# Kernel tuning notes

Measured on AMD Instinct MI355X. Metric: run time of the kernel, lower is better.

## Reference

```python
import jax, jax.numpy as jnp
import numpy as np

CODEBOOK_SIZE = 1024
CODEBOOK_DIM = 64
COMMITMENT_WEIGHT = 0.25
DECAY = 0.99
EPS = 1e-5


def setup_inputs() -> dict:
    key = jax.random.key(0)
    k1, k2, k3 = jax.random.split(key, 3)
    B, D, T = 32, CODEBOOK_DIM, 4096
    z = jax.random.normal(k1, (B, D, T), dtype=jnp.float32)
    embedding = jax.random.normal(k2, (CODEBOOK_SIZE, CODEBOOK_DIM), dtype=jnp.float32)
    cluster_size = jnp.zeros((CODEBOOK_SIZE,), dtype=jnp.float32)
    embed_avg = jax.random.normal(k3, (CODEBOOK_SIZE, CODEBOOK_DIM), dtype=jnp.float32)
    return {"z": z, "embedding": embedding, "cluster_size": cluster_size, "embed_avg": embed_avg}


def reference(z, embedding, cluster_size, embed_avg):
    # z: [B, D, T]; embedding/embed_avg: [K, D]; cluster_size: [K]
    B, D, T = z.shape
    K = embedding.shape[0]
    z_flat = jnp.transpose(z, (0, 2, 1)).reshape(-1, D)  # [N, D], N = B*T

    # squared-euclidean distances via expansion (matches torch cdist expansion)
    dist = (
        jnp.sum(z_flat * z_flat, axis=1, keepdims=True)
        + jnp.sum(embedding * embedding, axis=1)
        - 2.0 * (z_flat @ embedding.T)
    )  # [N, K]
    indices = jnp.argmin(dist, axis=1)  # [N] int

    # EMA updates (training path). one_hot.sum(0) -> segment count; one_hot.T @ z_flat -> segment sum
    counts = jax.ops.segment_sum(jnp.ones(z_flat.shape[0], dtype=z_flat.dtype), indices, num_segments=K)
    new_cluster_size = cluster_size * DECAY + (1.0 - DECAY) * counts
    embed_sum = jax.ops.segment_sum(z_flat, indices, num_segments=K)  # [K, D]
    new_embed_avg = embed_avg * DECAY + (1.0 - DECAY) * embed_sum
    n = jnp.sum(new_cluster_size)
    smoothed = (new_cluster_size + EPS) / (n + K * EPS) * n  # Laplace smoothing
    new_embedding = new_embed_avg / smoothed[:, None]  # [K, D]

    # quantize with the *updated* codebook (as in the torch in-place update)
    z_q_flat = new_embedding[indices]  # [N, D] gather
    loss = COMMITMENT_WEIGHT * jnp.mean((z_flat - jax.lax.stop_gradient(z_q_flat)) ** 2)
    # straight-through estimator
    z_q_flat = z_flat + jax.lax.stop_gradient(z_q_flat - z_flat)
    z_q = jnp.transpose(z_q_flat.reshape(B, T, D), (0, 2, 1))  # [B, D, T]
    return z_q, loss, indices.reshape(B, T)
```

## Files before the change

kernel.cpp:

```cpp
#include <hip/hip_runtime.h>

#define N_PTS 131072
#define TD 4096
#define DD 64
#define KK 1024
#define MARGIN_TH 2e-3f

typedef short bf16x8 __attribute__((ext_vector_type(8)));
typedef float f32x4  __attribute__((ext_vector_type(4)));

__device__ inline unsigned short f2bf(float f) {
    unsigned u = __float_as_uint(f);
    unsigned r = u + 0x7FFFu + ((u >> 16) & 1u);
    return (unsigned short)(r >> 16);
}
__device__ inline float bf2f(unsigned short h) {
    return __uint_as_float(((unsigned)h) << 16);
}

__device__ inline void gload_lds16(const unsigned short* g, unsigned short* l) {
    __builtin_amdgcn_global_load_lds(
        (const __attribute__((address_space(1))) unsigned int*)g,
        (__attribute__((address_space(3))) unsigned int*)l, 16, 0, 0);
}

__global__ __launch_bounds__(256) void vq_prep(const float* __restrict__ z,
                                               unsigned short* __restrict__ zh,
                                               unsigned short* __restrict__ zl)
{
    __shared__ float tile[64][65];
    const int tid = threadIdx.x;
    const int b = blockIdx.x >> 6;
    const int t0 = (blockIdx.x & 63) * 64;

    const int d = tid >> 2, tq = tid & 3;
#pragma unroll
    for (int it = 0; it < 4; ++it) {
        const int tt = tq * 16 + it * 4;
        const float4 v = *(const float4*)(z + ((size_t)b * DD + d) * TD + t0 + tt);
        tile[d][tt] = v.x; tile[d][tt + 1] = v.y; tile[d][tt + 2] = v.z; tile[d][tt + 3] = v.w;
    }
    __syncthreads();

    const int p = tid >> 2, dg = tid & 3;
    bf16x8 h0, h1, l0, l1;
#pragma unroll
    for (int j = 0; j < 8; ++j) {
        const float v0 = -tile[dg * 16 + j][p];
        const unsigned short a = f2bf(v0);
        h0[j] = (short)a; l0[j] = (short)f2bf(v0 - bf2f(a));
        const float v1 = -tile[dg * 16 + 8 + j][p];
        const unsigned short c = f2bf(v1);
        h1[j] = (short)c; l1[j] = (short)f2bf(v1 - bf2f(c));
    }
    const size_t o = ((size_t)(b * TD + t0 + p)) * DD + dg * 16;
    *(bf16x8*)(zh + o) = h0;
    *(bf16x8*)(zh + o + 8) = h1;
    *(bf16x8*)(zl + o) = l0;
    *(bf16x8*)(zl + o + 8) = l1;
}

__global__ __launch_bounds__(256) void vq_eprep(const float* __restrict__ emb,
                                                unsigned short* __restrict__ efh,
                                                unsigned short* __restrict__ efl,
                                                float* __restrict__ halfnorm)
{
    const int k = blockIdx.x * 256 + threadIdx.x;
    if (k >= KK) return;
    const int t = k >> 4, col = k & 15;
    const float* e = emb + (size_t)k * DD;
    double s = 0.0;
#pragma unroll
    for (int d = 0; d < DD; ++d) {
        const float v = e[d];
        const double dv = (double)v;
        s = fma(dv, dv, s);
        const unsigned short h = f2bf(v);
        const int q = d >> 3, j = d & 7;
        const size_t pos = (size_t)t * 1024 + (q >> 2) * 512 + ((q & 3) * 16 + col) * 8 + j;
        efh[pos] = h;
        efl[pos] = f2bf(v - bf2f(h));
    }
    halfnorm[k] = (float)(0.5 * s);
}

__global__ __launch_bounds__(512, 4) void vq_screen_mfma(
    const unsigned short* __restrict__ zh, const unsigned short* __restrict__ zl,
    const unsigned short* __restrict__ efh, const unsigned short* __restrict__ efl,
    const float* __restrict__ hn,
    int* __restrict__ idx_ws, float* __restrict__ ind_out,
    int* __restrict__ nflag, int* __restrict__ flags, int* __restrict__ hist)
{
    __shared__ __align__(16) unsigned short tiles[16][2048];

    const int tid  = threadIdx.x;
    const int lane = tid & 63;
    const int wv   = tid >> 6;
    const int quad = lane >> 4;
    const int col  = lane & 15;
    const int loff = lane * 8;
    const int pbase = blockIdx.x * 256 + wv * 32;

    const bf16x8* pA0h = (const bf16x8*)(zh + (size_t)(pbase + col) * DD + quad * 8);
    const bf16x8* pA0l = (const bf16x8*)(zl + (size_t)(pbase + col) * DD + quad * 8);
    const bf16x8* pA1h = (const bf16x8*)(zh + (size_t)(pbase + 16 + col) * DD + quad * 8);
    const bf16x8* pA1l = (const bf16x8*)(zl + (size_t)(pbase + 16 + col) * DD + quad * 8);
    const bf16x8 A0h0 = pA0h[0], A0h1 = pA0h[4];
    const bf16x8 A0l0 = pA0l[0], A0l1 = pA0l[4];
    const bf16x8 A1h0 = pA1h[0], A1h1 = pA1h[4];
    const bf16x8 A1l0 = pA1l[0], A1l1 = pA1l[4];

    float best0[4]  = {1e30f, 1e30f, 1e30f, 1e30f};
    float best20[4] = {1e30f, 1e30f, 1e30f, 1e30f};
    int   bidx0[4]  = {0, 0, 0, 0};
    float best1[4]  = {1e30f, 1e30f, 1e30f, 1e30f};
    float best21[4] = {1e30f, 1e30f, 1e30f, 1e30f};
    int   bidx1[4]  = {0, 0, 0, 0};

    for (int Q = 0; Q < 4; ++Q) {
        __syncthreads();

#pragma unroll
        for (int k = 0; k < 8; ++k) {
            const int T = Q * 16 + wv * 2 + (k >> 2);
            const unsigned short* src =
                ((k & 2) ? efl : efh) + (size_t)T * 1024 + (k & 1) * 512 + loff;
            unsigned short* dst =
                &tiles[0][0] + (wv * 2 + (k >> 2)) * 2048 + (k & 3) * 512 + loff;
            gload_lds16(src, dst);
        }
        asm volatile("s_waitcnt vmcnt(0)" ::: "memory");
        __syncthreads();

#pragma unroll 2
        for (int tt = 0; tt < 16; ++tt) {
            const unsigned short* buf = &tiles[tt][0];
            const bf16x8 Bh0 = *(const bf16x8*)(buf + loff);
            const bf16x8 Bh1 = *(const bf16x8*)(buf + 512 + loff);
            const bf16x8 Bl0 = *(const bf16x8*)(buf + 1024 + loff);
            const bf16x8 Bl1 = *(const bf16x8*)(buf + 1536 + loff);
            const int tg = Q * 16 + tt;
            const float chn = hn[tg * 16 + col];

            f32x4 p0 = {chn, chn, chn, chn}, q0 = {0.f, 0.f, 0.f, 0.f};
            f32x4 p1 = {chn, chn, chn, chn}, q1 = {0.f, 0.f, 0.f, 0.f};
            p0 = __builtin_amdgcn_mfma_f32_16x16x32_bf16(A0h0, Bh0, p0, 0, 0, 0);
            p1 = __builtin_amdgcn_mfma_f32_16x16x32_bf16(A1h0, Bh0, p1, 0, 0, 0);
            q0 = __builtin_amdgcn_mfma_f32_16x16x32_bf16(A0l0, Bh0, q0, 0, 0, 0);
            q1 = __builtin_amdgcn_mfma_f32_16x16x32_bf16(A1l0, Bh0, q1, 0, 0, 0);
            p0 = __builtin_amdgcn_mfma_f32_16x16x32_bf16(A0h1, Bh1, p0, 0, 0, 0);
            p1 = __builtin_amdgcn_mfma_f32_16x16x32_bf16(A1h1, Bh1, p1, 0, 0, 0);
            q0 = __builtin_amdgcn_mfma_f32_16x16x32_bf16(A0l1, Bh1, q0, 0, 0, 0);
            q1 = __builtin_amdgcn_mfma_f32_16x16x32_bf16(A1l1, Bh1, q1, 0, 0, 0);
            p0 = __builtin_amdgcn_mfma_f32_16x16x32_bf16(A0h0, Bl0, p0, 0, 0, 0);
            p1 = __builtin_amdgcn_mfma_f32_16x16x32_bf16(A1h0, Bl0, p1, 0, 0, 0);
            p0 = __builtin_amdgcn_mfma_f32_16x16x32_bf16(A0h1, Bl1, p0, 0, 0, 0);
            p1 = __builtin_amdgcn_mfma_f32_16x16x32_bf16(A1h1, Bl1, p1, 0, 0, 0);

            const int code = tg * 16 + col;
#pragma unroll
            for (int r = 0; r < 4; ++r) {
                const float s0 = p0[r] + q0[r];
                best20[r] = __builtin_amdgcn_fmed3f(best0[r], best20[r], s0);
                if (s0 < best0[r]) { best0[r] = s0; bidx0[r] = code; }
                const float s1 = p1[r] + q1[r];
                best21[r] = __builtin_amdgcn_fmed3f(best1[r], best21[r], s1);
                if (s1 < best1[r]) { best1[r] = s1; bidx1[r] = code; }
            }
        }
    }

#pragma unroll
    for (int off = 1; off < 16; off <<= 1) {
#pragma unroll
        for (int r = 0; r < 4; ++r) {
            {
                const float ob  = __shfl_xor(best0[r],  off, 64);
                const float ob2 = __shfl_xor(best20[r], off, 64);
                const int   oi  = __shfl_xor(bidx0[r],  off, 64);
                const float nb2 = fminf(fminf(best20[r], ob2), fmaxf(best0[r], ob));
                if (ob < best0[r]) { best0[r] = ob; bidx0[r] = oi; }
                best20[r] = nb2;
            }
            {
                const float ob  = __shfl_xor(best1[r],  off, 64);
                const float ob2 = __shfl_xor(best21[r], off, 64);
                const int   oi  = __shfl_xor(bidx1[r],  off, 64);
                const float nb2 = fminf(fminf(best21[r], ob2), fmaxf(best1[r], ob));
                if (ob < best1[r]) { best1[r] = ob; bidx1[r] = oi; }
                best21[r] = nb2;
            }
        }
    }

    if (col == 0) {
#pragma unroll
        for (int r = 0; r < 4; ++r) {
            const int n0 = pbase + quad * 4 + r;
            idx_ws[n0] = bidx0[r];
            ind_out[n0] = (float)bidx0[r];
            atomicAdd(&hist[bidx0[r]], 1);
            if (best20[r] - best0[r] < MARGIN_TH) {
                const int pos = atomicAdd(nflag, 1);
                flags[pos] = n0;
            }
            const int n1 = pbase + 16 + quad * 4 + r;
            idx_ws[n1] = bidx1[r];
            ind_out[n1] = (float)bidx1[r];
            atomicAdd(&hist[bidx1[r]], 1);
            if (best21[r] - best1[r] < MARGIN_TH) {
                const int pos = atomicAdd(nflag, 1);
                flags[pos] = n1;
            }
        }
    }
}

__global__ __launch_bounds__(256) void vq_fallback(
    const float* __restrict__ z, const float* __restrict__ emb,
    int* __restrict__ idx_ws, float* __restrict__ ind_out,
    const int* __restrict__ nflag, const int* __restrict__ flags,
    int* __restrict__ hist)
{
    __shared__ float zs[4][DD];
    const int total = *nflag;
    const int lane = threadIdx.x & 63;
    const int wid = threadIdx.x >> 6;
    const int gw = blockIdx.x * 4 + wid;

    for (int i = gw; i < total; i += gridDim.x * 4) {
        const int n = flags[i];
        const int b = n >> 12, t = n & 4095;
        zs[wid][lane] = z[((size_t)b * DD + lane) * TD + t];
        __builtin_amdgcn_s_waitcnt(0);
        double best = 1e300;
        int bi = KK;
        for (int kc = 0; kc < KK / 64; ++kc) {
            const int k = kc * 64 + lane;
            const float4* e = (const float4*)(emb + (size_t)k * DD);
            double dot = 0.0, nn = 0.0;
#pragma unroll
            for (int j = 0; j < 16; ++j) {
                float4 ev = e[j];
                double e0 = (double)ev.x, e1 = (double)ev.y, e2 = (double)ev.z, e3 = (double)ev.w;
                nn = fma(e0, e0, fma(e1, e1, fma(e2, e2, fma(e3, e3, nn))));
                dot = fma((double)zs[wid][4 * j + 0], e0,
                      fma((double)zs[wid][4 * j + 1], e1,
                      fma((double)zs[wid][4 * j + 2], e2,
                      fma((double)zs[wid][4 * j + 3], e3, dot))));
            }
            double s = 0.5 * nn - dot;
            if (s < best || (s == best && k < bi)) { best = s; bi = k; }
        }
        for (int off = 32; off > 0; off >>= 1) {
            double os = __shfl_down(best, off, 64);
            int oi = __shfl_down(bi, off, 64);
            if (os < best || (os == best && oi < bi)) { best = os; bi = oi; }
        }
        if (lane == 0) {
            const int old = idx_ws[n];
            if (bi != old) {
                idx_ws[n] = bi;
                ind_out[n] = (float)bi;
                atomicAdd(&hist[old], -1);
                atomicAdd(&hist[bi], 1);
            }
        }
    }
}

__global__ __launch_bounds__(1024) void vq_prefix_smo(
    const int* __restrict__ hist, const float* __restrict__ cs,
    int* __restrict__ cursor, float* __restrict__ rsmo)
{
    __shared__ int tmp[KK];
    __shared__ double dred[KK];
    const int k = threadIdx.x;
    const int c = hist[k];
    tmp[k] = c;
    const double ncs = 0.99 * (double)cs[k] + 0.01 * (double)c;
    dred[k] = ncs;
    __syncthreads();
    for (int off = 1; off < KK; off <<= 1) {
        int u = (k >= off) ? tmp[k - off] : 0;
        __syncthreads();
        tmp[k] += u;
        __syncthreads();
    }
    cursor[k] = tmp[k] - c;
    for (int s = 512; s > 0; s >>= 1) {
        if (k < s) dred[k] += dred[k + s];
        __syncthreads();
    }
    const double nsum = dred[0];
    const double smo = (ncs + 1e-5) / (nsum + (double)KK * 1e-5) * nsum;
    rsmo[k] = (float)(1.0 / smo);
}

__global__ __launch_bounds__(256) void vq_scatter(const int* __restrict__ idx_ws,
                                                  int* __restrict__ cursor, int* __restrict__ order)
{
    const int n = blockIdx.x * 256 + threadIdx.x;
    const int bi = idx_ws[n];
    const int pos = atomicAdd(&cursor[bi], 1);
    order[pos] = n;
}

__global__ __launch_bounds__(256) void vq_esum2(
    const unsigned short* __restrict__ zh, const unsigned short* __restrict__ zl,
    const int* __restrict__ idx_ws, const int* __restrict__ order,
    float* __restrict__ esum)
{
    const int tid = threadIdx.x;
    const int lane = tid & 63;
    const int w = tid >> 6;
    const int base = blockIdx.x * 256 + w * 64;

    const int pid_l = order[base + lane];
    const int code_l = idx_ws[pid_l];

    float v[64];
#pragma unroll
    for (int j = 0; j < 64; ++j) {
        const int pj = __shfl(pid_l, j, 64);
        const size_t o = (size_t)pj * DD + lane;
        v[j] = bf2f(zh[o]) + bf2f(zl[o]);
    }

    float racc = 0.f;
    int cur = __shfl(code_l, 0, 64);
#pragma unroll
    for (int j = 0; j < 64; ++j) {
        const int cj = __shfl(code_l, j, 64);
        if (cj != cur) {
            atomicAdd(&esum[(size_t)cur * DD + lane], -racc);
            racc = 0.f;
            cur = cj;
        }
        racc += v[j];
    }
    atomicAdd(&esum[(size_t)cur * DD + lane], -racc);
}

__global__ __launch_bounds__(256) void vq_newE(
    const float* __restrict__ avg, const float* __restrict__ esum,
    const float* __restrict__ rsmo, float* __restrict__ newE)
{
    const int j = blockIdx.x * 256 + threadIdx.x;
    newE[j] = (float)((0.99 * (double)avg[j] + 0.01 * (double)esum[j]) * (double)rsmo[j >> 6]);
}

__global__ __launch_bounds__(256) void vq_gather_loss(
    const float* __restrict__ z, const float* __restrict__ newE,
    const int* __restrict__ idx_ws, float* __restrict__ zq_out,
    double* __restrict__ loss_acc, int* __restrict__ done_cnt,
    float* __restrict__ loss_out)
{
    const int tid = threadIdx.x;
    const int n = blockIdx.x * 256 + tid;
    const int b = n >> 12;
    const int t = n & 4095;
    const float* zb = z + ((size_t)b * DD) * TD + t;
    float* ob = zq_out + ((size_t)b * DD) * TD + t;
    const int bi = idx_ws[n];
    const float* e = newE + (size_t)bi * DD;
    double acc = 0.0;
#pragma unroll
    for (int d = 0; d < DD; ++d) {
        float q = e[d];
        float zv = zb[(size_t)d * TD];
        ob[(size_t)d * TD] = q;
        float df = zv - q;
        acc = fma((double)df, (double)df, acc);
    }
    for (int off = 32; off > 0; off >>= 1) acc += __shfl_down(acc, off, 64);
    __shared__ double wsum[4];
    const int wid = tid >> 6, lane = tid & 63;
    if (lane == 0) wsum[wid] = acc;
    __syncthreads();
    if (tid == 0) {
        atomicAdd(loss_acc, wsum[0] + wsum[1] + wsum[2] + wsum[3]);
        __threadfence();
        const int prev = atomicAdd(done_cnt, 1);
        if (prev == gridDim.x - 1) {
            __threadfence();
            *loss_out = (float)(0.25 * (*loss_acc) / (double)(N_PTS * DD));
        }
    }
}

extern "C" void kernel_launch(void* const* d_in, const int* in_sizes, int n_in,
                              void* d_out, int out_size, void* d_ws, size_t ws_size,
                              hipStream_t stream) {
    const float* z    = (const float*)d_in[0];
    const float* emb  = (const float*)d_in[1];
    const float* cs   = (const float*)d_in[2];
    const float* avg  = (const float*)d_in[3];

    float* out      = (float*)d_out;
    float* zq_out   = out;
    float* loss_out = out + 8388608;
    float* ind_out  = out + 8388609;

    unsigned short* zh = (unsigned short*)d_out;
    unsigned short* zl = (unsigned short*)((char*)d_out + 16777216);

    char* ws = (char*)d_ws;
    int*            idx_ws   = (int*)ws;
    float*          newE     = (float*)(ws + 524288);
    float*          esum     = (float*)(ws + 786432);
    int*            hist     = (int*)(ws + 1048576);
    int*            nflag    = (int*)(ws + 1052672);
    int*            done_cnt = (int*)(ws + 1052676);
    double*         loss_acc = (double*)(ws + 1052680);
    float*          halfnorm = (float*)(ws + 1052688);
    int*            cursor   = (int*)(ws + 1056784);
    int*            flags    = (int*)(ws + 1060880);
    int*            order    = (int*)(ws + 1585168);
    unsigned short* efh      = (unsigned short*)(ws + 2109456);
    unsigned short* efl      = (unsigned short*)(ws + 2240528);
    float*          rsmo     = (float*)(ws + 2371600);

    hipMemsetAsync(ws + 786432, 0, 266256, stream);

    vq_prep<<<2048, 256, 0, stream>>>(z, zh, zl);
    vq_eprep<<<4, 256, 0, stream>>>(emb, efh, efl, halfnorm);
    vq_screen_mfma<<<512, 512, 0, stream>>>(zh, zl, efh, efl, halfnorm,
                                            idx_ws, ind_out, nflag, flags, hist);
    vq_fallback<<<128, 256, 0, stream>>>(z, emb, idx_ws, ind_out, nflag, flags, hist);
    vq_prefix_smo<<<1, 1024, 0, stream>>>(hist, cs, cursor, rsmo);
    vq_scatter<<<N_PTS / 256, 256, 0, stream>>>(idx_ws, cursor, order);
    vq_esum2<<<N_PTS / 256, 256, 0, stream>>>(zh, zl, idx_ws, order, esum);
    vq_newE<<<256, 256, 0, stream>>>(avg, esum, rsmo, newE);
    vq_gather_loss<<<N_PTS / 256, 256, 0, stream>>>(z, newE, idx_ws, zq_out,
                                                    loss_acc, done_cnt, loss_out);
}
```

Baseline: 334.3 us.

## Give each wave 64 points so codebook tiles are reused across four MFMA tiles

Result: no change. 339.7 us (+1.6%).

```diff
diff --git a/kernel.cpp b/kernel.cpp
--- a/kernel.cpp
+++ b/kernel.cpp
@@ -84,7 +84,7 @@
     halfnorm[k] = (float)(0.5 * s);
 }
 
-__global__ __launch_bounds__(512, 4) void vq_screen_mfma(
+__global__ __launch_bounds__(256, 2) void vq_screen_mfma(
     const unsigned short* __restrict__ zh, const unsigned short* __restrict__ zl,
     const unsigned short* __restrict__ efh, const unsigned short* __restrict__ efl,
     const float* __restrict__ hn,
@@ -92,6 +92,7 @@
     int* __restrict__ nflag, int* __restrict__ flags, int* __restrict__ hist)
 {
     __shared__ __align__(16) unsigned short tiles[16][2048];
+    __shared__ float hns[KK];
 
     const int tid  = threadIdx.x;
     const int lane = tid & 63;
@@ -99,40 +100,38 @@
     const int quad = lane >> 4;
     const int col  = lane & 15;
     const int loff = lane * 8;
-    const int pbase = blockIdx.x * 256 + wv * 32;
-
-    const bf16x8* pA0h = (const bf16x8*)(zh + (size_t)(pbase + col) * DD + quad * 8);
-    const bf16x8* pA0l = (const bf16x8*)(zl + (size_t)(pbase + col) * DD + quad * 8);
-    const bf16x8* pA1h = (const bf16x8*)(zh + (size_t)(pbase + 16 + col) * DD + quad * 8);
-    const bf16x8* pA1l = (const bf16x8*)(zl + (size_t)(pbase + 16 + col) * DD + quad * 8);
-    const bf16x8 A0h0 = pA0h[0], A0h1 = pA0h[4];
-    const bf16x8 A0l0 = pA0l[0], A0l1 = pA0l[4];
-    const bf16x8 A1h0 = pA1h[0], A1h1 = pA1h[4];
-    const bf16x8 A1l0 = pA1l[0], A1l1 = pA1l[4];
-
-    float best0[4]  = {1e30f, 1e30f, 1e30f, 1e30f};
-    float best20[4] = {1e30f, 1e30f, 1e30f, 1e30f};
-    int   bidx0[4]  = {0, 0, 0, 0};
-    float best1[4]  = {1e30f, 1e30f, 1e30f, 1e30f};
-    float best21[4] = {1e30f, 1e30f, 1e30f, 1e30f};
-    int   bidx1[4]  = {0, 0, 0, 0};
+    const int pbase = blockIdx.x * 256 + wv * 64;
+
+    bf16x8 Ah0[4], Ah1[4], Al0[4], Al1[4];
+#pragma unroll
+    for (int pt = 0; pt < 4; ++pt) {
+        const bf16x8* ph = (const bf16x8*)(zh + (size_t)(pbase + pt * 16 + col) * DD + quad * 8);
+        const bf16x8* pl = (const bf16x8*)(zl + (size_t)(pbase + pt * 16 + col) * DD + quad * 8);
+        Ah0[pt] = ph[0]; Ah1[pt] = ph[4];
+        Al0[pt] = pl[0]; Al1[pt] = pl[4];
+    }
+
+    ((float4*)hns)[tid] = ((const float4*)hn)[tid];
+
+    float best[4][4], best2[4][4];
+    int   bidx[4][4];
+#pragma unroll
+    for (int pt = 0; pt < 4; ++pt)
+#pragma unroll
+        for (int r = 0; r < 4; ++r) { best[pt][r] = 1e30f; best2[pt][r] = 1e30f; bidx[pt][r] = 0; }
+
+    const unsigned short* sg = (tid < 128 ? efh : efl) + (tid & 127) * 8;
 
     for (int Q = 0; Q < 4; ++Q) {
         __syncthreads();
 
 #pragma unroll
-        for (int k = 0; k < 8; ++k) {
-            const int T = Q * 16 + wv * 2 + (k >> 2);
-            const unsigned short* src =
-                ((k & 2) ? efl : efh) + (size_t)T * 1024 + (k & 1) * 512 + loff;
-            unsigned short* dst =
-                &tiles[0][0] + (wv * 2 + (k >> 2)) * 2048 + (k & 3) * 512 + loff;
-            gload_lds16(src, dst);
-        }
+        for (int k = 0; k < 16; ++k)
+            gload_lds16(sg + (size_t)(Q * 16 + k) * 1024, &tiles[k][0] + tid * 8);
         asm volatile("s_waitcnt vmcnt(0)" ::: "memory");
         __syncthreads();
 
-#pragma unroll 2
+#pragma unroll 4
         for (int tt = 0; tt < 16; ++tt) {
             const unsigned short* buf = &tiles[tt][0];
             const bf16x8 Bh0 = *(const bf16x8*)(buf + loff);
@@ -140,79 +139,75 @@
             const bf16x8 Bl0 = *(const bf16x8*)(buf + 1024 + loff);
             const bf16x8 Bl1 = *(const bf16x8*)(buf + 1536 + loff);
             const int tg = Q * 16 + tt;
-            const float chn = hn[tg * 16 + col];
-
-            f32x4 p0 = {chn, chn, chn, chn}, q0 = {0.f, 0.f, 0.f, 0.f};
-            f32x4 p1 = {chn, chn, chn, chn}, q1 = {0.f, 0.f, 0.f, 0.f};
-            p0 = __builtin_amdgcn_mfma_f32_16x16x32_bf16(A0h0, Bh0, p0, 0, 0, 0);
-            p1 = __builtin_amdgcn_mfma_f32_16x16x32_bf16(A1h0, Bh0, p1, 0, 0, 0);
-            q0 = __builtin_amdgcn_mfma_f32_16x16x32_bf16(A0l0, Bh0, q0, 0, 0, 0);
-            q1 = __builtin_amdgcn_mfma_f32_16x16x32_bf16(A1l0, Bh0, q1, 0, 0, 0);
-            p0 = __builtin_amdgcn_mfma_f32_16x16x32_bf16(A0h1, Bh1, p0, 0, 0, 0);
-            p1 = __builtin_amdgcn_mfma_f32_16x16x32_bf16(A1h1, Bh1, p1, 0, 0, 0);
-            q0 = __builtin_amdgcn_mfma_f32_16x16x32_bf16(A0l1, Bh1, q0, 0, 0, 0);
-            q1 = __builtin_amdgcn_mfma_f32_16x16x32_bf16(A1l1, Bh1, q1, 0, 0, 0);
-            p0 = __builtin_amdgcn_mfma_f32_16x16x32_bf16(A0h0, Bl0, p0, 0, 0, 0);
-            p1 = __builtin_amdgcn_mfma_f32_16x16x32_bf16(A1h0, Bl0, p1, 0, 0, 0);
-            p0 = __builtin_amdgcn_mfma_f32_16x16x32_bf16(A0h1, Bl1, p0, 0, 0, 0);
-            p1 = __builtin_amdgcn_mfma_f32_16x16x32_bf16(A1h1, Bl1, p1, 0, 0, 0);
+            const float chn = hns[tg * 16 + col];
+
+            f32x4 p[4], q[4];
+#pragma unroll
+            for (int pt = 0; pt < 4; ++pt) {
+                p[pt] = (f32x4){chn, chn, chn, chn};
+                q[pt] = (f32x4){0.f, 0.f, 0.f, 0.f};
+            }
+#pragma unroll
+            for (int pt = 0; pt < 4; ++pt)
+                p[pt] = __builtin_amdgcn_mfma_f32_16x16x32_bf16(Ah0[pt], Bh0, p[pt], 0, 0, 0);
+#pragma unroll
+            for (int pt = 0; pt < 4; ++pt)
+                q[pt] = __builtin_amdgcn_mfma_f32_16x16x32_bf16(Al0[pt], Bh0, q[pt], 0, 0, 0);
+#pragma unroll
+            for (int pt = 0; pt < 4; ++pt)
+                p[pt] = __builtin_amdgcn_mfma_f32_16x16x32_bf16(Ah1[pt], Bh1, p[pt], 0, 0, 0);
+#pragma unroll
+            for (int pt = 0; pt < 4; ++pt)
+                q[pt] = __builtin_amdgcn_mfma_f32_16x16x32_bf16(Al1[pt], Bh1, q[pt], 0, 0, 0);
+#pragma unroll
+            for (int pt = 0; pt < 4; ++pt)
+                p[pt] = __builtin_amdgcn_mfma_f32_16x16x32_bf16(Ah0[pt], Bl0, p[pt], 0, 0, 0);
+#pragma unroll
+            for (int pt = 0; pt < 4; ++pt)
+                p[pt] = __builtin_amdgcn_mfma_f32_16x16x32_bf16(Ah1[pt], Bl1, p[pt], 0, 0, 0);
 
             const int code = tg * 16 + col;
 #pragma unroll
+            for (int pt = 0; pt < 4; ++pt)
+#pragma unroll
+                for (int r = 0; r < 4; ++r) {
+                    const float s = p[pt][r] + q[pt][r];
+                    best2[pt][r] = __builtin_amdgcn_fmed3f(best[pt][r], best2[pt][r], s);
+                    bidx[pt][r] = (s < best[pt][r]) ? code : bidx[pt][r];
+                    best[pt][r] = fminf(best[pt][r], s);
+                }
+        }
+    }
+
+#pragma unroll
+    for (int off = 1; off < 16; off <<= 1) {
+#pragma unroll
+        for (int pt = 0; pt < 4; ++pt)
+#pragma unroll
             for (int r = 0; r < 4; ++r) {
-                const float s0 = p0[r] + q0[r];
-                best20[r] = __builtin_amdgcn_fmed3f(best0[r], best20[r], s0);
-                if (s0 < best0[r]) { best0[r] = s0; bidx0[r] = code; }
-                const float s1 = p1[r] + q1[r];
-                best21[r] = __builtin_amdgcn_fmed3f(best1[r], best21[r], s1);
-                if (s1 < best1[r]) { best1[r] = s1; bidx1[r] = code; }
+                const float ob  = __shfl_xor(best[pt][r],  off, 64);
+                const float ob2 = __shfl_xor(best2[pt][r], off, 64);
+                const int   oi  = __shfl_xor(bidx[pt][r],  off, 64);
+                const float nb2 = fminf(fminf(best2[pt][r], ob2), fmaxf(best[pt][r], ob));
+                if (ob < best[pt][r]) { best[pt][r] = ob; bidx[pt][r] = oi; }
+                best2[pt][r] = nb2;
             }
-        }
-    }
-
-#pragma unroll
-    for (int off = 1; off < 16; off <<= 1) {
-#pragma unroll
-        for (int r = 0; r < 4; ++r) {
-            {
-                const float ob  = __shfl_xor(best0[r],  off, 64);
-                const float ob2 = __shfl_xor(best20[r], off, 64);
-                const int   oi  = __shfl_xor(bidx0[r],  off, 64);
-                const float nb2 = fminf(fminf(best20[r], ob2), fmaxf(best0[r], ob));
-                if (ob < best0[r]) { best0[r] = ob; bidx0[r] = oi; }
-                best20[r] = nb2;
+    }
+
+    if (col == 0) {
+#pragma unroll
+        for (int pt = 0; pt < 4; ++pt)
+#pragma unroll
+            for (int r = 0; r < 4; ++r) {
+                const int n0 = pbase + pt * 16 + quad * 4 + r;
+                idx_ws[n0] = bidx[pt][r];
+                ind_out[n0] = (float)bidx[pt][r];
+                atomicAdd(&hist[bidx[pt][r]], 1);
+                if (best2[pt][r] - best[pt][r] < MARGIN_TH) {
+                    const int pos = atomicAdd(nflag, 1);
+                    flags[pos] = n0;
+                }
             }
-            {
-                const float ob  = __shfl_xor(best1[r],  off, 64);
-                const float ob2 = __shfl_xor(best21[r], off, 64);
-                const int   oi  = __shfl_xor(bidx1[r],  off, 64);
-                const float nb2 = fminf(fminf(best21[r], ob2), fmaxf(best1[r], ob));
-                if (ob < best1[r]) { best1[r] = ob; bidx1[r] = oi; }
-                best21[r] = nb2;
-            }
-        }
-    }
-
-    if (col == 0) {
-#pragma unroll
-        for (int r = 0; r < 4; ++r) {
-            const int n0 = pbase + quad * 4 + r;
-            idx_ws[n0] = bidx0[r];
-            ind_out[n0] = (float)bidx0[r];
-            atomicAdd(&hist[bidx0[r]], 1);
-            if (best20[r] - best0[r] < MARGIN_TH) {
-                const int pos = atomicAdd(nflag, 1);
-                flags[pos] = n0;
-            }
-            const int n1 = pbase + 16 + quad * 4 + r;
-            idx_ws[n1] = bidx1[r];
-            ind_out[n1] = (float)bidx1[r];
-            atomicAdd(&hist[bidx1[r]], 1);
-            if (best21[r] - best1[r] < MARGIN_TH) {
-                const int pos = atomicAdd(nflag, 1);
-                flags[pos] = n1;
-            }
-        }
     }
 }
 
@@ -425,7 +420,7 @@
 
     vq_prep<<<2048, 256, 0, stream>>>(z, zh, zl);
     vq_eprep<<<4, 256, 0, stream>>>(emb, efh, efl, halfnorm);
-    vq_screen_mfma<<<512, 512, 0, stream>>>(zh, zl, efh, efl, halfnorm,
+    vq_screen_mfma<<<512, 256, 0, stream>>>(zh, zl, efh, efl, halfnorm,
                                             idx_ws, ind_out, nflag, flags, hist);
     vq_fallback<<<128, 256, 0, stream>>>(z, emb, idx_ws, ind_out, nflag, flags, hist);
     vq_prefix_smo<<<1, 1024, 0, stream>>>(hist, cs, cursor, rsmo);
```
